# Optimization experiments

Measured on AMD Instinct MI355X. Metric: run time of the kernel, lower is better.

Reference implementation:

```python
import jax, jax.numpy as jnp
import numpy as np

B, L, D, H = 256, 256, 128, 256
IMPUTE_WEIGHT = 1.0


def setup_inputs() -> dict:
    key = jax.random.key(0)
    ks = jax.random.split(key, 20)
    s = 0.05
    inp = {
        "values": jax.random.normal(ks[0], (B, L, D), jnp.float32),
        "masks": jax.random.randint(ks[1], (B, L, D), 0, 2).astype(jnp.float32),
        "deltas": jax.random.uniform(ks[2], (B, L, D), jnp.float32),
        "eval_masks": jax.random.randint(ks[3], (B, L, D), 0, 2).astype(jnp.float32),
        "td_h_W": jax.random.normal(ks[4], (H, D), jnp.float32) * s,
        "td_h_b": jax.random.normal(ks[5], (H,), jnp.float32) * s,
        "td_x_w": jax.random.normal(ks[6], (D,), jnp.float32) * s,  # diag of TemporalDecay(diag=True)
        "td_x_b": jax.random.normal(ks[7], (D,), jnp.float32) * s,
        "hist_W": jax.random.normal(ks[8], (D, H), jnp.float32) * s,
        "hist_b": jax.random.normal(ks[9], (D,), jnp.float32) * s,
        "feat_W": jax.random.normal(ks[10], (D, D), jnp.float32) * s,
        "feat_b": jax.random.normal(ks[11], (D,), jnp.float32) * s,
        "wc_W": jax.random.normal(ks[12], (D, 2 * D), jnp.float32) * s,
        "wc_b": jax.random.normal(ks[13], (D,), jnp.float32) * s,
        "W_ih": jax.random.normal(ks[14], (4 * H, 2 * D), jnp.float32) * s,
        "W_hh": jax.random.normal(ks[15], (4 * H, H), jnp.float32) * s,
        "b_ih": jax.random.normal(ks[16], (4 * H,), jnp.float32) * s,
        "b_hh": jax.random.normal(ks[17], (4 * H,), jnp.float32) * s,
    }
    return inp


def _rits_forward(values, masks, deltas, eval_masks,
                  td_h_W, td_h_b, td_x_w, td_x_b,
                  hist_W, hist_b, feat_W, feat_b,
                  wc_W, wc_b, W_ih, W_hh, b_ih, b_hh):
    feat_mask = 1.0 - jnp.eye(D, dtype=values.dtype)  # zero diagonal
    Wf = feat_W * feat_mask

    def step(carry, xs):
        h, c, loss = carry
        x, m, d, me = xs  # each (B, D)
        gamma_h = jnp.exp(-jax.nn.relu(d @ td_h_W.T + td_h_b))   # (B, H)
        gamma_x = jnp.exp(-jax.nn.relu(d * td_x_w + td_x_b))      # (B, D) diag linear
        h = h * gamma_h
        x_h = h @ hist_W.T + hist_b                               # (B, D)
        x_c = m * x + (1.0 - m) * x_h
        z_h = x_c @ Wf.T + feat_b                                 # (B, D)
        alpha = jnp.concatenate([gamma_x, m], axis=1) @ wc_W.T + wc_b
        c_h = alpha * z_h + (1.0 - alpha) * x_h
        c_c = m * x + (1.0 - m) * c_h
        loss = loss + jnp.sum(jnp.abs(c_c - x) * me) / (jnp.sum(me) + 1e-5)
        inputs = jnp.concatenate([c_c, m], axis=1)                # (B, 2D)
        gates = inputs @ W_ih.T + b_ih + h @ W_hh.T + b_hh        # (B, 4H)
        i, f, g, o = jnp.split(gates, 4, axis=1)
        i, f, o = jax.nn.sigmoid(i), jax.nn.sigmoid(f), jax.nn.sigmoid(o)
        g = jnp.tanh(g)
        c = f * c + i * g
        h = o * jnp.tanh(c)
        return (h, c, loss), c_c

    h0 = jnp.zeros((values.shape[0], H), values.dtype)
    c0 = jnp.zeros((values.shape[0], H), values.dtype)
    loss0 = jnp.zeros((), values.dtype)
    xs = (jnp.swapaxes(values, 0, 1), jnp.swapaxes(masks, 0, 1),
          jnp.swapaxes(deltas, 0, 1), jnp.swapaxes(eval_masks, 0, 1))  # (L, B, D)
    (_, _, loss), imps = jax.lax.scan(step, (h0, c0, loss0), xs)
    imputations = jnp.swapaxes(imps, 0, 1)  # (B, L, D)
    return imputations, loss * IMPUTE_WEIGHT


def reference(values, masks, deltas, eval_masks,
              td_h_W, td_h_b, td_x_w, td_x_b,
              hist_W, hist_b, feat_W, feat_b,
              wc_W, wc_b, W_ih, W_hh, b_ih, b_hh):
    return _rits_forward(values, masks, deltas, eval_masks,
                         td_h_W, td_h_b, td_x_w, td_x_b,
                         hist_W, hist_b, feat_W, feat_b,
                         wc_W, wc_b, W_ih, W_hh, b_ih, b_hh)
```

## Files before the change

### kernel.cpp

```cpp
#include <hip/hip_runtime.h>
#include <math.h>


namespace {
constexpr int Bn = 256, Ln = 256, Dn = 128, Hn = 256;
constexpr long LD = (long)Ln * Dn;

constexpr int OFF_LOSS  = 0;
constexpr int OFF_DEN   = 256;
constexpr int OFF_BIASG = 2048;
constexpr int OFF_WG    = 8192;
constexpr int OFF_HISTP = 1056768;
constexpr int OFF_TDHP  = 1122304;
constexpr int OFF_WFP   = 1187840;
constexpr int OFF_WCP   = 1220608;
}

typedef _Float16 h2f __attribute__((ext_vector_type(2)));
typedef unsigned int uint32;

__device__ __forceinline__ float fdot2(uint32 a, uint32 b, float c) {
  return __builtin_amdgcn_fdot2(__builtin_bit_cast(h2f, a),
                                __builtin_bit_cast(h2f, b), c, false);
}
__device__ __forceinline__ uint32 packf16(float a, float b) {
  h2f p; p[0] = (_Float16)a; p[1] = (_Float16)b;
  return __builtin_bit_cast(uint32, p);
}
__device__ __forceinline__ unsigned short f16u(float a) {
  _Float16 h = (_Float16)a; return __builtin_bit_cast(unsigned short, h);
}

__global__ void rits_prep(const float* __restrict__ td_h_W,
                          const float* __restrict__ hist_W,
                          const float* __restrict__ feat_W,
                          const float* __restrict__ wc_W,
                          const float* __restrict__ W_ih,
                          const float* __restrict__ W_hh,
                          const float* __restrict__ b_ih,
                          const float* __restrict__ b_hh,
                          const float* __restrict__ evalm,
                          char* __restrict__ wsb) {
  const int blk = blockIdx.x, tid = threadIdx.x;
  if (blk < 1248) {
    int idx = blk * 256 + tid;
    if (idx < 262144) {
      int kp = idx >> 11, rem = idx & 2047, jj = rem >> 3, s8 = rem & 7;
      const float* src = (s8 < 4) ? W_ih : W_hh;
      int q = s8 & 3;
      const float* row = src + (size_t)(q * 256 + jj) * 256 + 2 * kp;
      ((uint32*)(wsb + OFF_WG))[idx] = packf16(row[0], row[1]);
    } else if (idx < 278528) {
      int i2 = idx - 262144, kp = i2 >> 7, d = i2 & 127;
      ((uint32*)(wsb + OFF_HISTP))[i2] =
          packf16(hist_W[d * 256 + 2 * kp], hist_W[d * 256 + 2 * kp + 1]);
    } else if (idx < 294912) {
      int i2 = idx - 278528, kp = i2 >> 8, h = i2 & 255;
      ((uint32*)(wsb + OFF_TDHP))[i2] =
          packf16(td_h_W[h * 128 + 2 * kp], td_h_W[h * 128 + 2 * kp + 1]);
    } else if (idx < 303104) {
      int i2 = idx - 294912, kp = i2 >> 7, d = i2 & 127;
      float a = (2 * kp == d) ? 0.f : feat_W[d * 128 + 2 * kp];
      float b = (2 * kp + 1 == d) ? 0.f : feat_W[d * 128 + 2 * kp + 1];
      ((uint32*)(wsb + OFF_WFP))[i2] = packf16(a, b);
    } else if (idx < 319488) {
      int i2 = idx - 303104, kp = i2 >> 7, d = i2 & 127;
      ((uint32*)(wsb + OFF_WCP))[i2] =
          packf16(wc_W[d * 256 + 2 * kp], wc_W[d * 256 + 2 * kp + 1]);
    }
  } else if (blk < 1252) {
    int i = (blk - 1248) * 256 + tid;
    int jj = i >> 2, q = i & 3;
    ((float*)(wsb + OFF_BIASG))[jj * 4 + q] =
        b_ih[q * 256 + jj] + b_hh[q * 256 + jj];
    if (blk == 1248 && tid == 0) *((float*)(wsb + OFF_LOSS)) = 0.f;
  } else {
    int t = blk - 1252;
    __shared__ float red[256];
    int d = tid & 127, g = tid >> 7;
    float s = 0.f;
    for (int b = g; b < 256; b += 2) s += evalm[(size_t)b * LD + t * 128 + d];
    red[tid] = s;
    __syncthreads();
    for (int o = 128; o > 0; o >>= 1) {
      if (tid < o) red[tid] += red[tid + o];
      __syncthreads();
    }
    if (tid == 0) ((float*)(wsb + OFF_DEN))[t] = red[0] + 1e-5f;
  }
}

__global__ __launch_bounds__(1024, 4) void rits_rec(
    const float* __restrict__ values, const float* __restrict__ masks,
    const float* __restrict__ deltas, const float* __restrict__ evalm,
    const float* __restrict__ td_h_b, const float* __restrict__ td_x_w,
    const float* __restrict__ td_x_b, const float* __restrict__ hist_b,
    const float* __restrict__ feat_b, const float* __restrict__ wc_b,
    char* __restrict__ wsb, float* __restrict__ outp) {
  __shared__ __align__(16) float scratch[8224];
  __shared__ float den_s[256], bg_s[1024], tdhb_s[256];
  __shared__ float txw_s[128], txb_s[128], hb_s[128], fb_s[128], wcb_s[128];
  __shared__ float hf[2][256], cst[2][256];
  __shared__ float xs[2][128], ms[2][128], es[2][128];
  __shared__ float xh_s[2][128], al_s[2][128];
  __shared__ __align__(8) unsigned short hdU16[128 * 4];
  __shared__ __align__(8) unsigned short cmU16[128 * 4];
  __shared__ __align__(8) unsigned short xcU16[64 * 4];
  __shared__ uint32 drP[64 * 2];
  __shared__ uint32 gxmP[128 * 2];

  const int tid = threadIdx.x;
  const size_t b0 = (size_t)blockIdx.x * 2;
  const uint32* hdU32 = (const uint32*)hdU16;
  const uint32* cmU32 = (const uint32*)cmU16;
  const uint32* xcU32 = (const uint32*)xcU16;
  const uint32* wg = (const uint32*)(wsb + OFF_WG);
  const uint4* histP4 = (const uint4*)(wsb + OFF_HISTP);
  const uint4* tdhP4 = (const uint4*)(wsb + OFF_TDHP);
  const uint4* wfP4 = (const uint4*)(wsb + OFF_WFP);
  const uint4* wcP4 = (const uint4*)(wsb + OFF_WCP);

  if (tid < 512) { ((float*)hf)[tid] = 0.f; ((float*)cst)[tid] = 0.f; }
  bg_s[tid] = ((const float*)(wsb + OFF_BIASG))[tid];
  if (tid < 256) {
    den_s[tid] = ((const float*)(wsb + OFF_DEN))[tid];
    tdhb_s[tid] = td_h_b[tid];
  } else if (tid < 384) txw_s[tid - 256] = td_x_w[tid - 256];
  else if (tid < 512) txb_s[tid - 384] = td_x_b[tid - 384];
  else if (tid < 640) hb_s[tid - 512] = hist_b[tid - 512];
  else if (tid < 768) fb_s[tid - 640] = feat_b[tid - 640];
  else if (tid < 896) wcb_s[tid - 768] = wc_b[tid - 768];
  __syncthreads();

  float lacc = 0.f;
  for (int t = 0; t < Ln; ++t) {
    const size_t base = b0 * LD + (size_t)t * 128;
    if (tid < 256) {
      int d = tid & 127, r = tid >> 7;
      size_t gi = base + (size_t)r * LD + d;
      xs[r][d] = values[gi];
      ms[r][d] = masks[gi];
      es[r][d] = evalm[gi];
    } else if (tid < 512) {
      int i = tid - 256, kp = i & 127, r = i >> 7;
      size_t gb = base + (size_t)r * LD;
      if (kp < 64) {
        float d0v = deltas[gb + 2 * kp], d1v = deltas[gb + 2 * kp + 1];
        drP[kp * 2 + r] = packf16(d0v, d1v);
        float g0 = __expf(-fmaxf(fmaf(d0v, txw_s[2 * kp], txb_s[2 * kp]), 0.f));
        float g1 = __expf(-fmaxf(fmaf(d1v, txw_s[2 * kp + 1], txb_s[2 * kp + 1]), 0.f));
        gxmP[kp * 2 + r] = packf16(g0, g1);
      } else {
        int k2 = kp - 64;
        gxmP[kp * 2 + r] = packf16(masks[gb + 2 * k2], masks[gb + 2 * k2 + 1]);
      }
    }
    __syncthreads();

    if (tid < 256) {
      int g = tid & 63, r = (tid >> 6) & 1, kq = tid >> 7;
      float4 a = {0.f, 0.f, 0.f, 0.f};
#pragma unroll 4
      for (int i = 0; i < 32; ++i) {
        int kp = kq * 32 + i;
        uint4 w = tdhP4[kp * 64 + g];
        uint32 dr = drP[kp * 2 + r];
        a.x = fdot2(dr, w.x, a.x); a.y = fdot2(dr, w.y, a.y);
        a.z = fdot2(dr, w.z, a.z); a.w = fdot2(dr, w.w, a.w);
      }
      ((float4*)(scratch + (kq * 2 + r) * 260))[g] = a;
    } else if (tid < 768) {
      int i0 = tid - 256, g = i0 & 31, r = (i0 >> 5) & 1, kq = i0 >> 6;
      float4 a = {0.f, 0.f, 0.f, 0.f};
#pragma unroll 4
      for (int i = 0; i < 16; ++i) {
        int kp = kq * 16 + i;
        uint4 w = wcP4[kp * 32 + g];
        uint32 gm = gxmP[kp * 2 + r];
        a.x = fdot2(gm, w.x, a.x); a.y = fdot2(gm, w.y, a.y);
        a.z = fdot2(gm, w.z, a.z); a.w = fdot2(gm, w.w, a.w);
      }
      ((float4*)(scratch + 1040 + (kq * 2 + r) * 132))[g] = a;
    }
    __syncthreads();

    if (tid < 512) {
      int h = tid & 255, r = tid >> 8;
      float s = scratch[r * 260 + h] + scratch[(2 + r) * 260 + h] + tdhb_s[h];
      float hd = hf[r][h] * __expf(-fmaxf(s, 0.f));
      hdU16[(h >> 1) * 4 + 2 * r + (h & 1)] = f16u(hd);
    } else if (tid < 768) {
      int i0 = tid - 512, d = i0 & 127, r = i0 >> 7;
      float s = wcb_s[d];
#pragma unroll
      for (int kq = 0; kq < 8; ++kq) s += scratch[1040 + (kq * 2 + r) * 132 + d];
      al_s[r][d] = s;
    }
    __syncthreads();

    if (tid < 512) {
      int g = tid & 31, r = (tid >> 5) & 1, kq = tid >> 6;
      float4 a = {0.f, 0.f, 0.f, 0.f};
#pragma unroll 4
      for (int i = 0; i < 16; ++i) {
        int kp = kq * 16 + i;
        uint4 w = histP4[kp * 32 + g];
        uint32 hd = hdU32[kp * 2 + r];
        a.x = fdot2(hd, w.x, a.x); a.y = fdot2(hd, w.y, a.y);
        a.z = fdot2(hd, w.z, a.z); a.w = fdot2(hd, w.w, a.w);
      }
      ((float4*)(scratch + (kq * 2 + r) * 132))[g] = a;
    }
    __syncthreads();

    if (tid < 256) {
      int d = tid & 127, r = tid >> 7;
      float xh = hb_s[d];
#pragma unroll
      for (int kq = 0; kq < 8; ++kq) xh += scratch[(kq * 2 + r) * 132 + d];
      xh_s[r][d] = xh;
      float mm = ms[r][d];
      float xc = mm * xs[r][d] + (1.f - mm) * xh;
      xcU16[(d >> 1) * 4 + 2 * r + (d & 1)] = f16u(xc);
    }
    __syncthreads();

    if (tid < 512) {
      int g = tid & 31, r = (tid >> 5) & 1, kq = tid >> 6;
      float4 a = {0.f, 0.f, 0.f, 0.f};
#pragma unroll 4
      for (int i = 0; i < 8; ++i) {
        int kp = kq * 8 + i;
        uint4 w = wfP4[kp * 32 + g];
        uint32 xc = xcU32[kp * 2 + r];
        a.x = fdot2(xc, w.x, a.x); a.y = fdot2(xc, w.y, a.y);
        a.z = fdot2(xc, w.z, a.z); a.w = fdot2(xc, w.w, a.w);
      }
      ((float4*)(scratch + (kq * 2 + r) * 132))[g] = a;
    }
    __syncthreads();

    if (tid < 256) {
      int d = tid & 127, r = tid >> 7;
      float z = fb_s[d];
#pragma unroll
      for (int kq = 0; kq < 8; ++kq) z += scratch[(kq * 2 + r) * 132 + d];
      float a = al_s[r][d], xh = xh_s[r][d];
      float ch = a * z + (1.f - a) * xh;
      float mm = ms[r][d], xv = xs[r][d];
      float cc = mm * xv + (1.f - mm) * ch;
      outp[base + (size_t)r * LD + d] = cc;
      lacc += (1.f - mm) * fabsf(ch - xv) * es[r][d] / den_s[t];
      cmU16[(d >> 1) * 4 + 2 * r + (d & 1)] = f16u(cc);
      cmU16[(64 + (d >> 1)) * 4 + 2 * r + (d & 1)] = f16u(mm);
    }
    __syncthreads();

    {
      int jj = tid & 255, kq = tid >> 8;
      int kp0 = kq * 32;
      const uint4* wp = (const uint4*)(wg + ((size_t)kp0 * 256 + jj) * 8);
      float a00 = 0, a01 = 0, a02 = 0, a03 = 0;
      float a10 = 0, a11 = 0, a12 = 0, a13 = 0;
#pragma unroll 4
      for (int i = 0; i < 32; ++i) {
        int kp = kp0 + i;
        uint4 wv = wp[0];
        uint4 wh = wp[1];
        wp += 512;
        uint32 c0 = cmU32[kp * 2 + 0], c1 = cmU32[kp * 2 + 1];
        uint32 h0 = hdU32[kp * 2 + 0], h1 = hdU32[kp * 2 + 1];
        a00 = fdot2(c0, wv.x, a00); a01 = fdot2(c0, wv.y, a01);
        a02 = fdot2(c0, wv.z, a02); a03 = fdot2(c0, wv.w, a03);
        a10 = fdot2(c1, wv.x, a10); a11 = fdot2(c1, wv.y, a11);
        a12 = fdot2(c1, wv.z, a12); a13 = fdot2(c1, wv.w, a13);
        a00 = fdot2(h0, wh.x, a00); a01 = fdot2(h0, wh.y, a01);
        a02 = fdot2(h0, wh.z, a02); a03 = fdot2(h0, wh.w, a03);
        a10 = fdot2(h1, wh.x, a10); a11 = fdot2(h1, wh.y, a11);
        a12 = fdot2(h1, wh.z, a12); a13 = fdot2(h1, wh.w, a13);
      }
      float* pg = scratch;
      pg[(kq * 8 + 0) * 257 + jj] = a00; pg[(kq * 8 + 1) * 257 + jj] = a01;
      pg[(kq * 8 + 2) * 257 + jj] = a02; pg[(kq * 8 + 3) * 257 + jj] = a03;
      pg[(kq * 8 + 4) * 257 + jj] = a10; pg[(kq * 8 + 5) * 257 + jj] = a11;
      pg[(kq * 8 + 6) * 257 + jj] = a12; pg[(kq * 8 + 7) * 257 + jj] = a13;
    }
    __syncthreads();

    if (tid < 256) {
      int jj = tid;
      const float* pg = scratch;
#pragma unroll
      for (int r = 0; r < 2; ++r) {
        float g0 = bg_s[jj * 4 + 0], g1 = bg_s[jj * 4 + 1];
        float g2 = bg_s[jj * 4 + 2], g3 = bg_s[jj * 4 + 3];
#pragma unroll
        for (int kq = 0; kq < 4; ++kq) {
          g0 += pg[(kq * 8 + r * 4 + 0) * 257 + jj];
          g1 += pg[(kq * 8 + r * 4 + 1) * 257 + jj];
          g2 += pg[(kq * 8 + r * 4 + 2) * 257 + jj];
          g3 += pg[(kq * 8 + r * 4 + 3) * 257 + jj];
        }
        float ig = 1.f / (1.f + __expf(-g0));
        float fg = 1.f / (1.f + __expf(-g1));
        float gg = tanhf(g2);
        float og = 1.f / (1.f + __expf(-g3));
        float c = fg * cst[r][jj] + ig * gg;
        cst[r][jj] = c;
        hf[r][jj] = og * tanhf(c);
      }
    }
    __syncthreads();
  }

  scratch[tid] = lacc;
  __syncthreads();
  for (int o = 512; o > 0; o >>= 1) {
    if (tid < o) scratch[tid] += scratch[tid + o];
    __syncthreads();
  }
  if (tid == 0) atomicAdd((float*)(wsb + OFF_LOSS), scratch[0]);
}

__global__ void rits_fin(const char* __restrict__ wsb, float* __restrict__ outp) {
  if (threadIdx.x == 0 && blockIdx.x == 0)
    outp[(size_t)Bn * LD] = *((const float*)(wsb + OFF_LOSS));
}

extern "C" void kernel_launch(void* const* d_in, const int* in_sizes, int n_in,
                              void* d_out, int out_size, void* d_ws,
                              size_t ws_size, hipStream_t stream) {
  const float* values = (const float*)d_in[0];
  const float* masks  = (const float*)d_in[1];
  const float* deltas = (const float*)d_in[2];
  const float* evalm  = (const float*)d_in[3];
  const float* td_h_W = (const float*)d_in[4];
  const float* td_h_b = (const float*)d_in[5];
  const float* td_x_w = (const float*)d_in[6];
  const float* td_x_b = (const float*)d_in[7];
  const float* hist_W = (const float*)d_in[8];
  const float* hist_b = (const float*)d_in[9];
  const float* feat_W = (const float*)d_in[10];
  const float* feat_b = (const float*)d_in[11];
  const float* wc_W   = (const float*)d_in[12];
  const float* wc_b   = (const float*)d_in[13];
  const float* W_ih   = (const float*)d_in[14];
  const float* W_hh   = (const float*)d_in[15];
  const float* b_ih   = (const float*)d_in[16];
  const float* b_hh   = (const float*)d_in[17];
  char* wsb = (char*)d_ws;
  float* outp = (float*)d_out;

  hipLaunchKernelGGL(rits_prep, dim3(1508), dim3(256), 0, stream, td_h_W,
                     hist_W, feat_W, wc_W, W_ih, W_hh, b_ih, b_hh, evalm, wsb);
  hipLaunchKernelGGL(rits_rec, dim3(128), dim3(1024), 0, stream, values, masks,
                     deltas, evalm, td_h_b, td_x_w, td_x_b, hist_b, feat_b,
                     wc_b, wsb, outp);
  hipLaunchKernelGGL(rits_fin, dim3(1), dim3(64), 0, stream, wsb, outp);
}
```

Before: 3.562 ms.

## Split each batch pair's recurrence across two blocks exchanging state via global flags

Launches two blocks per batch pair, each owning half of the hidden units (H split) for the temporal-decay, history projection and LSTM gate matvecs. Each step the blocks exchange their decayed hidden halves and partial x_h sums through a global workspace, using release/acquire flags with a bounded spin. This doubles the number of active CUs on the serial recurrence and halves per-block weight streaming. The cost is a cross-block global-memory handshake every time step, and the scheme relies on both partner blocks being co-resident.

```diff
diff --git a/kernel.cpp b/kernel.cpp
--- a/kernel.cpp
+++ b/kernel.cpp
@@ -14,10 +14,13 @@
 constexpr int OFF_TDHP  = 1122304;
 constexpr int OFF_WFP   = 1187840;
 constexpr int OFF_WCP   = 1220608;
+constexpr int OFF_EXCH  = 1310720;
+constexpr int OFF_FLAG  = 2097152;
 }
 
 typedef _Float16 h2f __attribute__((ext_vector_type(2)));
 typedef unsigned int uint32;
+typedef unsigned long long uint64;
 
 __device__ __forceinline__ float fdot2(uint32 a, uint32 b, float c) {
   return __builtin_amdgcn_fdot2(__builtin_bit_cast(h2f, a),
@@ -74,7 +77,7 @@
     ((float*)(wsb + OFF_BIASG))[jj * 4 + q] =
         b_ih[q * 256 + jj] + b_hh[q * 256 + jj];
     if (blk == 1248 && tid == 0) *((float*)(wsb + OFF_LOSS)) = 0.f;
-  } else {
+  } else if (blk < 1508) {
     int t = blk - 1252;
     __shared__ float red[256];
     int d = tid & 127, g = tid >> 7;
@@ -87,6 +90,8 @@
       __syncthreads();
     }
     if (tid == 0) ((float*)(wsb + OFF_DEN))[t] = red[0] + 1e-5f;
+  } else {
+    for (int i = tid; i < 4096; i += 256) ((uint32*)(wsb + OFF_FLAG))[i] = 0u;
   }
 }
 
@@ -97,11 +102,12 @@
     const float* __restrict__ td_x_b, const float* __restrict__ hist_b,
     const float* __restrict__ feat_b, const float* __restrict__ wc_b,
     char* __restrict__ wsb, float* __restrict__ outp) {
-  __shared__ __align__(16) float scratch[8224];
-  __shared__ float den_s[256], bg_s[1024], tdhb_s[256];
+  __shared__ __align__(16) float scratch[8448];
+  __shared__ float den_s[256], bg_s[512], tdhb_s[128];
   __shared__ float txw_s[128], txb_s[128], hb_s[128], fb_s[128], wcb_s[128];
-  __shared__ float hf[2][256], cst[2][256];
+  __shared__ float hf[2][128], cst[2][128];
   __shared__ float xs[2][128], ms[2][128], es[2][128];
+  __shared__ float xhp[2][2][128];
   __shared__ float xh_s[2][128], al_s[2][128];
   __shared__ __align__(8) unsigned short hdU16[128 * 4];
   __shared__ __align__(8) unsigned short cmU16[128 * 4];
@@ -110,7 +116,10 @@
   __shared__ uint32 gxmP[128 * 2];
 
   const int tid = threadIdx.x;
-  const size_t b0 = (size_t)blockIdx.x * 2;
+  const int bid = blockIdx.x;
+  const int sh = bid >> 7;
+  const int pair = bid & 127;
+  const size_t b0 = (size_t)pair * 2;
   const uint32* hdU32 = (const uint32*)hdU16;
   const uint32* cmU32 = (const uint32*)cmU16;
   const uint32* xcU32 = (const uint32*)xcU16;
@@ -119,22 +128,31 @@
   const uint4* tdhP4 = (const uint4*)(wsb + OFF_TDHP);
   const uint4* wfP4 = (const uint4*)(wsb + OFF_WFP);
   const uint4* wcP4 = (const uint4*)(wsb + OFF_WCP);
-
-  if (tid < 512) { ((float*)hf)[tid] = 0.f; ((float*)cst)[tid] = 0.f; }
-  bg_s[tid] = ((const float*)(wsb + OFF_BIASG))[tid];
-  if (tid < 256) {
-    den_s[tid] = ((const float*)(wsb + OFF_DEN))[tid];
-    tdhb_s[tid] = td_h_b[tid];
-  } else if (tid < 384) txw_s[tid - 256] = td_x_w[tid - 256];
-  else if (tid < 512) txb_s[tid - 384] = td_x_b[tid - 384];
-  else if (tid < 640) hb_s[tid - 512] = hist_b[tid - 512];
-  else if (tid < 768) fb_s[tid - 640] = feat_b[tid - 640];
-  else if (tid < 896) wcb_s[tid - 768] = wc_b[tid - 768];
+  char* exch = wsb + OFF_EXCH;
+  unsigned int* myf = (unsigned int*)(wsb + OFF_FLAG + ((pair << 1) | sh) * 64);
+  unsigned int* pf  = (unsigned int*)(wsb + OFF_FLAG + ((pair << 1) | (sh ^ 1)) * 64);
+
+  if (tid < 512) bg_s[tid] = ((const float*)(wsb + OFF_BIASG))[sh * 512 + tid];
+  else if (tid < 768) den_s[tid - 512] = ((const float*)(wsb + OFF_DEN))[tid - 512];
+  else if (tid < 896) tdhb_s[tid - 768] = td_h_b[(sh << 7) + (tid - 768)];
+  else txw_s[tid - 896] = td_x_w[tid - 896];
+  if (tid < 128) txb_s[tid] = td_x_b[tid];
+  else if (tid < 256) hb_s[tid - 128] = hist_b[tid - 128];
+  else if (tid < 384) fb_s[tid - 256] = feat_b[tid - 256];
+  else if (tid < 512) wcb_s[tid - 384] = wc_b[tid - 384];
+  else {
+    int i = tid - 512;
+    if (i < 256) ((float*)hf)[i] = 0.f;
+    else ((float*)cst)[i - 256] = 0.f;
+  }
   __syncthreads();
 
   float lacc = 0.f;
   for (int t = 0; t < Ln; ++t) {
     const size_t base = b0 * LD + (size_t)t * 128;
+    uint64* myp = (uint64*)(exch + ((((pair << 1) | sh) << 1) | (t & 1)) * 1536);
+    uint64* pp  = (uint64*)(exch + ((((pair << 1) | (sh ^ 1)) << 1) | (t & 1)) * 1536);
+
     if (tid < 256) {
       int d = tid & 127, r = tid >> 7;
       size_t gi = base + (size_t)r * LD + d;
@@ -158,17 +176,18 @@
     __syncthreads();
 
     if (tid < 256) {
-      int g = tid & 63, r = (tid >> 6) & 1, kq = tid >> 7;
+      int g = tid & 31, r = (tid >> 5) & 1, kq = tid >> 6;
+      int gg = (sh << 5) + g;
       float4 a = {0.f, 0.f, 0.f, 0.f};
 #pragma unroll 4
-      for (int i = 0; i < 32; ++i) {
-        int kp = kq * 32 + i;
-        uint4 w = tdhP4[kp * 64 + g];
+      for (int i = 0; i < 16; ++i) {
+        int kp = kq * 16 + i;
+        uint4 w = tdhP4[kp * 64 + gg];
         uint32 dr = drP[kp * 2 + r];
         a.x = fdot2(dr, w.x, a.x); a.y = fdot2(dr, w.y, a.y);
         a.z = fdot2(dr, w.z, a.z); a.w = fdot2(dr, w.w, a.w);
       }
-      ((float4*)(scratch + (kq * 2 + r) * 260))[g] = a;
+      ((float4*)(scratch + (kq * 2 + r) * 132))[g] = a;
     } else if (tid < 768) {
       int i0 = tid - 256, g = i0 & 31, r = (i0 >> 5) & 1, kq = i0 >> 6;
       float4 a = {0.f, 0.f, 0.f, 0.f};
@@ -180,21 +199,24 @@
         a.x = fdot2(gm, w.x, a.x); a.y = fdot2(gm, w.y, a.y);
         a.z = fdot2(gm, w.z, a.z); a.w = fdot2(gm, w.w, a.w);
       }
-      ((float4*)(scratch + 1040 + (kq * 2 + r) * 132))[g] = a;
-    }
-    __syncthreads();
-
-    if (tid < 512) {
-      int h = tid & 255, r = tid >> 8;
-      float s = scratch[r * 260 + h] + scratch[(2 + r) * 260 + h] + tdhb_s[h];
-      float hd = hf[r][h] * __expf(-fmaxf(s, 0.f));
-      hdU16[(h >> 1) * 4 + 2 * r + (h & 1)] = f16u(hd);
-    } else if (tid < 768) {
+      ((float4*)(scratch + 1056 + (kq * 2 + r) * 132))[g] = a;
+    }
+    __syncthreads();
+
+    if (tid < 256) {
+      int hl = tid & 127, r = tid >> 7;
+      float ssum = tdhb_s[hl];
+#pragma unroll
+      for (int kq = 0; kq < 4; ++kq) ssum += scratch[(kq * 2 + r) * 132 + hl];
+      float hd = hf[r][hl] * __expf(-fmaxf(ssum, 0.f));
+      int hg = (sh << 7) | hl;
+      hdU16[(hg >> 1) * 4 + 2 * r + (hg & 1)] = f16u(hd);
+    } else if (tid >= 512 && tid < 768) {
       int i0 = tid - 512, d = i0 & 127, r = i0 >> 7;
-      float s = wcb_s[d];
+      float ssum = wcb_s[d];
 #pragma unroll
-      for (int kq = 0; kq < 8; ++kq) s += scratch[1040 + (kq * 2 + r) * 132 + d];
-      al_s[r][d] = s;
+      for (int kq = 0; kq < 8; ++kq) ssum += scratch[1056 + (kq * 2 + r) * 132 + d];
+      al_s[r][d] = ssum;
     }
     __syncthreads();
 
@@ -202,22 +224,61 @@
       int g = tid & 31, r = (tid >> 5) & 1, kq = tid >> 6;
       float4 a = {0.f, 0.f, 0.f, 0.f};
 #pragma unroll 4
-      for (int i = 0; i < 16; ++i) {
-        int kp = kq * 16 + i;
+      for (int i = 0; i < 8; ++i) {
+        int kp = (sh << 6) + kq * 8 + i;
         uint4 w = histP4[kp * 32 + g];
         uint32 hd = hdU32[kp * 2 + r];
         a.x = fdot2(hd, w.x, a.x); a.y = fdot2(hd, w.y, a.y);
         a.z = fdot2(hd, w.z, a.z); a.w = fdot2(hd, w.w, a.w);
       }
       ((float4*)(scratch + (kq * 2 + r) * 132))[g] = a;
+    } else if (tid < 576) {
+      int i = tid - 512;
+      uint64 v = ((const uint64*)hdU16)[(sh << 6) + i];
+      __hip_atomic_store(myp + i, v, __ATOMIC_RELAXED, __HIP_MEMORY_SCOPE_AGENT);
     }
     __syncthreads();
 
     if (tid < 256) {
       int d = tid & 127, r = tid >> 7;
-      float xh = hb_s[d];
+      float xo = 0.f;
 #pragma unroll
-      for (int kq = 0; kq < 8; ++kq) xh += scratch[(kq * 2 + r) * 132 + d];
+      for (int kq = 0; kq < 8; ++kq) xo += scratch[(kq * 2 + r) * 132 + d];
+      xhp[sh][r][d] = xo;
+      __hip_atomic_store((uint32*)myp + 128 + (r << 7) + d,
+                         __builtin_bit_cast(uint32, xo),
+                         __ATOMIC_RELAXED, __HIP_MEMORY_SCOPE_AGENT);
+    }
+    __syncthreads();
+
+    if (tid == 0) {
+      __hip_atomic_store(myf, (unsigned)(t + 1), __ATOMIC_RELEASE,
+                         __HIP_MEMORY_SCOPE_AGENT);
+      unsigned guard = 0;
+      while (__hip_atomic_load(pf, __ATOMIC_ACQUIRE,
+                               __HIP_MEMORY_SCOPE_AGENT) < (unsigned)(t + 1)) {
+        if (++guard > (1u << 22)) break;
+      }
+    }
+    __syncthreads();
+
+    if (tid < 192) {
+      uint64 v = __hip_atomic_load(pp + tid, __ATOMIC_RELAXED,
+                                   __HIP_MEMORY_SCOPE_AGENT);
+      if (tid < 64) {
+        ((uint64*)hdU16)[((sh ^ 1) << 6) + tid] = v;
+      } else {
+        int j = tid - 64;
+        int r = j >> 6, d2 = (j & 63) << 1;
+        xhp[sh ^ 1][r][d2] = __builtin_bit_cast(float, (uint32)v);
+        xhp[sh ^ 1][r][d2 + 1] = __builtin_bit_cast(float, (uint32)(v >> 32));
+      }
+    }
+    __syncthreads();
+
+    if (tid < 256) {
+      int d = tid & 127, r = tid >> 7;
+      float xh = xhp[0][r][d] + xhp[1][r][d] + hb_s[d];
       xh_s[r][d] = xh;
       float mm = ms[r][d];
       float xc = mm * xs[r][d] + (1.f - mm) * xh;
@@ -249,21 +310,24 @@
       float ch = a * z + (1.f - a) * xh;
       float mm = ms[r][d], xv = xs[r][d];
       float cc = mm * xv + (1.f - mm) * ch;
-      outp[base + (size_t)r * LD + d] = cc;
-      lacc += (1.f - mm) * fabsf(ch - xv) * es[r][d] / den_s[t];
+      if (r == sh) {
+        outp[base + (size_t)r * LD + d] = cc;
+        lacc += (1.f - mm) * fabsf(ch - xv) * es[r][d] / den_s[t];
+      }
       cmU16[(d >> 1) * 4 + 2 * r + (d & 1)] = f16u(cc);
       cmU16[(64 + (d >> 1)) * 4 + 2 * r + (d & 1)] = f16u(mm);
     }
     __syncthreads();
 
     {
-      int jj = tid & 255, kq = tid >> 8;
-      int kp0 = kq * 32;
-      const uint4* wp = (const uint4*)(wg + ((size_t)kp0 * 256 + jj) * 8);
+      int jj = tid & 127, kq = tid >> 7;
+      int jg = (sh << 7) | jj;
+      int kp0 = kq * 16;
+      const uint4* wp = (const uint4*)(wg + ((size_t)kp0 * 256 + jg) * 8);
       float a00 = 0, a01 = 0, a02 = 0, a03 = 0;
       float a10 = 0, a11 = 0, a12 = 0, a13 = 0;
 #pragma unroll 4
-      for (int i = 0; i < 32; ++i) {
+      for (int i = 0; i < 16; ++i) {
         int kp = kp0 + i;
         uint4 wv = wp[0];
         uint4 wh = wp[1];
@@ -280,35 +344,30 @@
         a12 = fdot2(h1, wh.z, a12); a13 = fdot2(h1, wh.w, a13);
       }
       float* pg = scratch;
-      pg[(kq * 8 + 0) * 257 + jj] = a00; pg[(kq * 8 + 1) * 257 + jj] = a01;
-      pg[(kq * 8 + 2) * 257 + jj] = a02; pg[(kq * 8 + 3) * 257 + jj] = a03;
-      pg[(kq * 8 + 4) * 257 + jj] = a10; pg[(kq * 8 + 5) * 257 + jj] = a11;
-      pg[(kq * 8 + 6) * 257 + jj] = a12; pg[(kq * 8 + 7) * 257 + jj] = a13;
-    }
-    __syncthreads();
-
-    if (tid < 256) {
-      int jj = tid;
-      const float* pg = scratch;
+      pg[(kq * 8 + 0) * 132 + jj] = a00; pg[(kq * 8 + 1) * 132 + jj] = a01;
+      pg[(kq * 8 + 2) * 132 + jj] = a02; pg[(kq * 8 + 3) * 132 + jj] = a03;
+      pg[(kq * 8 + 4) * 132 + jj] = a10; pg[(kq * 8 + 5) * 132 + jj] = a11;
+      pg[(kq * 8 + 6) * 132 + jj] = a12; pg[(kq * 8 + 7) * 132 + jj] = a13;
+    }
+    __syncthreads();
+
+    if (tid < 256) {
+      int jj = tid & 127, r = tid >> 7;
+      float g0 = bg_s[jj * 4 + 0], g1 = bg_s[jj * 4 + 1];
+      float g2 = bg_s[jj * 4 + 2], g3 = bg_s[jj * 4 + 3];
 #pragma unroll
-      for (int r = 0; r < 2; ++r) {
-        float g0 = bg_s[jj * 4 + 0], g1 = bg_s[jj * 4 + 1];
-        float g2 = bg_s[jj * 4 + 2], g3 = bg_s[jj * 4 + 3];
-#pragma unroll
-        for (int kq = 0; kq < 4; ++kq) {
-          g0 += pg[(kq * 8 + r * 4 + 0) * 257 + jj];
-          g1 += pg[(kq * 8 + r * 4 + 1) * 257 + jj];
-          g2 += pg[(kq * 8 + r * 4 + 2) * 257 + jj];
-          g3 += pg[(kq * 8 + r * 4 + 3) * 257 + jj];
-        }
-        float ig = 1.f / (1.f + __expf(-g0));
-        float fg = 1.f / (1.f + __expf(-g1));
-        float gg = tanhf(g2);
-        float og = 1.f / (1.f + __expf(-g3));
-        float c = fg * cst[r][jj] + ig * gg;
-        cst[r][jj] = c;
-        hf[r][jj] = og * tanhf(c);
-      }
+      for (int kq = 0; kq < 8; ++kq) {
+        int bix = (kq * 8 + r * 4) * 132 + jj;
+        g0 += scratch[bix]; g1 += scratch[bix + 132];
+        g2 += scratch[bix + 264]; g3 += scratch[bix + 396];
+      }
+      float ig = 1.f / (1.f + __expf(-g0));
+      float fg = 1.f / (1.f + __expf(-g1));
+      float gg = tanhf(g2);
+      float og = 1.f / (1.f + __expf(-g3));
+      float c = fg * cst[r][jj] + ig * gg;
+      cst[r][jj] = c;
+      hf[r][jj] = og * tanhf(c);
     }
     __syncthreads();
   }
@@ -351,9 +410,9 @@
   char* wsb = (char*)d_ws;
   float* outp = (float*)d_out;
 
-  hipLaunchKernelGGL(rits_prep, dim3(1508), dim3(256), 0, stream, td_h_W,
+  hipLaunchKernelGGL(rits_prep, dim3(1509), dim3(256), 0, stream, td_h_W,
                      hist_W, feat_W, wc_W, W_ih, W_hh, b_ih, b_hh, evalm, wsb);
-  hipLaunchKernelGGL(rits_rec, dim3(128), dim3(1024), 0, stream, values, masks,
+  hipLaunchKernelGGL(rits_rec, dim3(256), dim3(1024), 0, stream, values, masks,
                      deltas, evalm, td_h_b, td_x_w, td_x_b, hist_b, feat_b,
                      wc_b, wsb, outp);
   hipLaunchKernelGGL(rits_fin, dim3(1), dim3(64), 0, stream, wsb, outp);
```

New measurement: 3.563 ms. No clear change (+0.0%).

## Split LSTM hidden dim across 4 cooperating blocks with global flag exchange

Applied to the files above, without the earlier changes.

Restructures the recurrent kernel so each group of 4 batch rows is handled by 4 blocks, each owning a quarter of the hidden units. The blocks exchange the decayed hidden state and alpha slices each timestep through global memory using release/acquire flags. Gate weights stay in registers and the hist/feat weights are cached in LDS. This cuts per-block weight traffic and spreads the work over 256 blocks. The cost is a cross-block spin-wait every step and the assumption that all 256 blocks are resident at once, which could deadlock or hit the guard timeout if they are not.

```diff
diff --git a/kernel.cpp b/kernel.cpp
--- a/kernel.cpp
+++ b/kernel.cpp
@@ -14,6 +14,8 @@
 constexpr int OFF_TDHP  = 1122304;
 constexpr int OFF_WFP   = 1187840;
 constexpr int OFF_WCP   = 1220608;
+constexpr int OFF_EXCH  = 1286144;
+constexpr int OFF_FLAG  = 1810432;
 }
 
 typedef _Float16 h2f __attribute__((ext_vector_type(2)));
@@ -26,9 +28,6 @@
 __device__ __forceinline__ uint32 packf16(float a, float b) {
   h2f p; p[0] = (_Float16)a; p[1] = (_Float16)b;
   return __builtin_bit_cast(uint32, p);
-}
-__device__ __forceinline__ unsigned short f16u(float a) {
-  _Float16 h = (_Float16)a; return __builtin_bit_cast(unsigned short, h);
 }
 
 __global__ void rits_prep(const float* __restrict__ td_h_W,
@@ -74,7 +73,7 @@
     ((float*)(wsb + OFF_BIASG))[jj * 4 + q] =
         b_ih[q * 256 + jj] + b_hh[q * 256 + jj];
     if (blk == 1248 && tid == 0) *((float*)(wsb + OFF_LOSS)) = 0.f;
-  } else {
+  } else if (blk < 1508) {
     int t = blk - 1252;
     __shared__ float red[256];
     int d = tid & 127, g = tid >> 7;
@@ -87,235 +86,278 @@
       __syncthreads();
     }
     if (tid == 0) ((float*)(wsb + OFF_DEN))[t] = red[0] + 1e-5f;
+  } else {
+    for (int i = tid; i < 4096; i += 256) ((uint32*)(wsb + OFF_FLAG))[i] = 0u;
   }
 }
 
-__global__ __launch_bounds__(1024, 4) void rits_rec(
+__global__ __launch_bounds__(512, 2) void rits_rec(
     const float* __restrict__ values, const float* __restrict__ masks,
     const float* __restrict__ deltas, const float* __restrict__ evalm,
     const float* __restrict__ td_h_b, const float* __restrict__ td_x_w,
     const float* __restrict__ td_x_b, const float* __restrict__ hist_b,
     const float* __restrict__ feat_b, const float* __restrict__ wc_b,
     char* __restrict__ wsb, float* __restrict__ outp) {
-  __shared__ __align__(16) float scratch[8224];
-  __shared__ float den_s[256], bg_s[1024], tdhb_s[256];
+  __shared__ uint32 histL[16384];
+  __shared__ uint32 wfL[8192];
+  __shared__ __align__(16) float scratch[4608];
+  __shared__ float al_s[4][128];
+  __shared__ float hf[4][64], cst[4][64];
+  __shared__ __align__(16) uint32 hdP[512];
+  __shared__ __align__(16) uint32 cmP[512];
+  __shared__ __align__(16) uint32 xcP[256];
+  __shared__ __align__(16) uint32 drP[256];
+  __shared__ __align__(16) uint32 gxmP[512];
+  __shared__ float bg_s[256];
+  __shared__ float tdhb_s[64];
   __shared__ float txw_s[128], txb_s[128], hb_s[128], fb_s[128], wcb_s[128];
-  __shared__ float hf[2][256], cst[2][256];
-  __shared__ float xs[2][128], ms[2][128], es[2][128];
-  __shared__ float xh_s[2][128], al_s[2][128];
-  __shared__ __align__(8) unsigned short hdU16[128 * 4];
-  __shared__ __align__(8) unsigned short cmU16[128 * 4];
-  __shared__ __align__(8) unsigned short xcU16[64 * 4];
-  __shared__ uint32 drP[64 * 2];
-  __shared__ uint32 gxmP[128 * 2];
 
   const int tid = threadIdx.x;
-  const size_t b0 = (size_t)blockIdx.x * 2;
-  const uint32* hdU32 = (const uint32*)hdU16;
-  const uint32* cmU32 = (const uint32*)cmU16;
-  const uint32* xcU32 = (const uint32*)xcU16;
+  const int bid = blockIdx.x;
+  const int sh = bid >> 6;
+  const int grp = bid & 63;
+  const size_t b0 = (size_t)grp * 4;
   const uint32* wg = (const uint32*)(wsb + OFF_WG);
-  const uint4* histP4 = (const uint4*)(wsb + OFF_HISTP);
-  const uint4* tdhP4 = (const uint4*)(wsb + OFF_TDHP);
-  const uint4* wfP4 = (const uint4*)(wsb + OFF_WFP);
-  const uint4* wcP4 = (const uint4*)(wsb + OFF_WCP);
-
-  if (tid < 512) { ((float*)hf)[tid] = 0.f; ((float*)cst)[tid] = 0.f; }
-  bg_s[tid] = ((const float*)(wsb + OFF_BIASG))[tid];
+  const uint32* tdhG = (const uint32*)(wsb + OFF_TDHP);
+  const uint32* wcG = (const uint32*)(wsb + OFF_WCP);
+  const float* denG = (const float*)(wsb + OFF_DEN);
+  char* exch = wsb + OFF_EXCH;
+  unsigned int* flg = (unsigned int*)(wsb + OFF_FLAG);
+
+  {
+    const uint4* hG = (const uint4*)(wsb + OFF_HISTP);
+#pragma unroll
+    for (int k = 0; k < 8; ++k) ((uint4*)histL)[k * 512 + tid] = hG[k * 512 + tid];
+    const uint4* fG = (const uint4*)(wsb + OFF_WFP);
+#pragma unroll
+    for (int k = 0; k < 4; ++k) ((uint4*)wfL)[k * 512 + tid] = fG[k * 512 + tid];
+  }
   if (tid < 256) {
-    den_s[tid] = ((const float*)(wsb + OFF_DEN))[tid];
-    tdhb_s[tid] = td_h_b[tid];
-  } else if (tid < 384) txw_s[tid - 256] = td_x_w[tid - 256];
-  else if (tid < 512) txb_s[tid - 384] = td_x_b[tid - 384];
-  else if (tid < 640) hb_s[tid - 512] = hist_b[tid - 512];
-  else if (tid < 768) fb_s[tid - 640] = feat_b[tid - 640];
-  else if (tid < 896) wcb_s[tid - 768] = wc_b[tid - 768];
+    bg_s[tid] = ((const float*)(wsb + OFF_BIASG))[(sh * 64 + (tid & 63)) * 4 + (tid >> 6)];
+  } else if (tid < 320) tdhb_s[tid - 256] = td_h_b[sh * 64 + (tid - 256)];
+  else if (tid < 448) txw_s[tid - 320] = td_x_w[tid - 320];
+  if (tid < 128) txb_s[tid] = td_x_b[tid];
+  else if (tid < 256) hb_s[tid - 128] = hist_b[tid - 128];
+  else if (tid < 384) fb_s[tid - 256] = feat_b[tid - 256];
+  else wcb_s[tid - 384] = wc_b[tid - 384];
+  if (tid < 256) ((float*)hf)[tid] = 0.f;
+  else ((float*)cst)[tid - 256] = 0.f;
+
+  const int dA = tid & 127, rA = tid >> 7;
+  const int hlB = tid & 63, kqB = (tid >> 6) & 7;
+  const int dlB = tid & 31, kqA = tid >> 5;
+  const int jjH = tid & 63, qhH = (tid >> 6) & 1, kqH = tid >> 7;
+  const int jg = sh * 64 + jjH;
+
+  uint2 wv_[32], wh_[32];
+#pragma unroll
+  for (int i = 0; i < 32; ++i) {
+    const uint32* p = wg + ((size_t)((kqH * 32 + i) * 256 + jg)) * 8 + 2 * qhH;
+    wv_[i] = *(const uint2*)p;
+    wh_[i] = *(const uint2*)(p + 4);
+  }
+  uint32 tw[8];
+#pragma unroll
+  for (int i = 0; i < 8; ++i) tw[i] = tdhG[(kqB * 8 + i) * 256 + sh * 64 + hlB];
+  uint32 cw[8];
+#pragma unroll
+  for (int i = 0; i < 8; ++i) cw[i] = wcG[(kqA * 8 + i) * 128 + sh * 32 + dlB];
   __syncthreads();
 
   float lacc = 0.f;
   for (int t = 0; t < Ln; ++t) {
     const size_t base = b0 * LD + (size_t)t * 128;
+    uint32* mypU = (uint32*)(exch + (size_t)(bid * 2 + (t & 1)) * 1024);
+
+    const size_t gi = base + (size_t)rA * LD + dA;
+    const float xv = values[gi];
+    const float mv = masks[gi];
+    const float ev = evalm[gi];
+    {
+      const size_t gb = base + (size_t)rA * LD;
+      if (dA < 64) {
+        float d0v = deltas[gb + 2 * dA], d1v = deltas[gb + 2 * dA + 1];
+        drP[dA * 4 + rA] = packf16(d0v, d1v);
+        float g0 = __expf(-fmaxf(fmaf(d0v, txw_s[2 * dA], txb_s[2 * dA]), 0.f));
+        float g1 = __expf(-fmaxf(fmaf(d1v, txw_s[2 * dA + 1], txb_s[2 * dA + 1]), 0.f));
+        gxmP[dA * 4 + rA] = packf16(g0, g1);
+      } else {
+        int k2 = dA - 64;
+        gxmP[dA * 4 + rA] = packf16(masks[gb + 2 * k2], masks[gb + 2 * k2 + 1]);
+      }
+    }
+    __syncthreads();
+
+    {
+      float ga0 = 0.f, ga1 = 0.f, ga2 = 0.f, ga3 = 0.f;
+#pragma unroll
+      for (int i = 0; i < 8; ++i) {
+        uint4 d4 = *(const uint4*)&drP[(kqB * 8 + i) * 4];
+        ga0 = fdot2(d4.x, tw[i], ga0); ga1 = fdot2(d4.y, tw[i], ga1);
+        ga2 = fdot2(d4.z, tw[i], ga2); ga3 = fdot2(d4.w, tw[i], ga3);
+      }
+      scratch[2304 + (kqB * 4 + 0) * 68 + hlB] = ga0;
+      scratch[2304 + (kqB * 4 + 1) * 68 + hlB] = ga1;
+      scratch[2304 + (kqB * 4 + 2) * 68 + hlB] = ga2;
+      scratch[2304 + (kqB * 4 + 3) * 68 + hlB] = ga3;
+      float aa0 = 0.f, aa1 = 0.f, aa2 = 0.f, aa3 = 0.f;
+#pragma unroll
+      for (int i = 0; i < 8; ++i) {
+        uint4 g4 = *(const uint4*)&gxmP[(kqA * 8 + i) * 4];
+        aa0 = fdot2(g4.x, cw[i], aa0); aa1 = fdot2(g4.y, cw[i], aa1);
+        aa2 = fdot2(g4.z, cw[i], aa2); aa3 = fdot2(g4.w, cw[i], aa3);
+      }
+      scratch[(kqA * 4 + 0) * 36 + dlB] = aa0;
+      scratch[(kqA * 4 + 1) * 36 + dlB] = aa1;
+      scratch[(kqA * 4 + 2) * 36 + dlB] = aa2;
+      scratch[(kqA * 4 + 3) * 36 + dlB] = aa3;
+    }
+    __syncthreads();
+
     if (tid < 256) {
-      int d = tid & 127, r = tid >> 7;
-      size_t gi = base + (size_t)r * LD + d;
-      xs[r][d] = values[gi];
-      ms[r][d] = masks[gi];
-      es[r][d] = evalm[gi];
-    } else if (tid < 512) {
-      int i = tid - 256, kp = i & 127, r = i >> 7;
-      size_t gb = base + (size_t)r * LD;
-      if (kp < 64) {
-        float d0v = deltas[gb + 2 * kp], d1v = deltas[gb + 2 * kp + 1];
-        drP[kp * 2 + r] = packf16(d0v, d1v);
-        float g0 = __expf(-fmaxf(fmaf(d0v, txw_s[2 * kp], txb_s[2 * kp]), 0.f));
-        float g1 = __expf(-fmaxf(fmaf(d1v, txw_s[2 * kp + 1], txb_s[2 * kp + 1]), 0.f));
-        gxmP[kp * 2 + r] = packf16(g0, g1);
-      } else {
-        int k2 = kp - 64;
-        gxmP[kp * 2 + r] = packf16(masks[gb + 2 * k2], masks[gb + 2 * k2 + 1]);
+      int hl = tid & 63, r = tid >> 6;
+      float s = tdhb_s[hl];
+#pragma unroll
+      for (int kq = 0; kq < 8; ++kq) s += scratch[2304 + (kq * 4 + r) * 68 + hl];
+      float hd = hf[r][hl] * __expf(-fmaxf(s, 0.f));
+      float hdo = __shfl_down(hd, 1);
+      if (!(hl & 1)) {
+        uint32 pv = packf16(hd, hdo);
+        int kpl = hl >> 1;
+        hdP[(sh * 32 + kpl) * 4 + r] = pv;
+        __hip_atomic_store(mypU + kpl * 4 + r, pv, __ATOMIC_RELAXED,
+                           __HIP_MEMORY_SCOPE_AGENT);
+      }
+    } else if (tid < 384) {
+      int i0 = tid - 256, dl = i0 & 31, r = i0 >> 5;
+      float s = wcb_s[sh * 32 + dl];
+#pragma unroll
+      for (int kq = 0; kq < 16; ++kq) s += scratch[(kq * 4 + r) * 36 + dl];
+      al_s[r][sh * 32 + dl] = s;
+      __hip_atomic_store(mypU + 128 + r * 32 + dl,
+                         __builtin_bit_cast(uint32, s),
+                         __ATOMIC_RELAXED, __HIP_MEMORY_SCOPE_AGENT);
+    }
+    __syncthreads();
+
+    if (tid == 0)
+      __hip_atomic_store(flg + bid * 16, (unsigned)(t + 1), __ATOMIC_RELEASE,
+                         __HIP_MEMORY_SCOPE_AGENT);
+    if (tid < 3) {
+      int ps = tid + (tid >= sh ? 1 : 0);
+      unsigned* pfp = flg + (ps * 64 + grp) * 16;
+      unsigned guard = 0;
+      while (__hip_atomic_load(pfp, __ATOMIC_ACQUIRE,
+                               __HIP_MEMORY_SCOPE_AGENT) < (unsigned)(t + 1)) {
+        if (++guard > (1u << 24)) break;
       }
     }
     __syncthreads();
 
     if (tid < 256) {
-      int g = tid & 63, r = (tid >> 6) & 1, kq = tid >> 7;
-      float4 a = {0.f, 0.f, 0.f, 0.f};
-#pragma unroll 4
+#pragma unroll
+      for (int p = 0; p < 3; ++p) {
+        int ps = p + (p >= sh ? 1 : 0);
+        const uint32* pq =
+            (const uint32*)(exch + (size_t)((ps * 64 + grp) * 2 + (t & 1)) * 1024);
+        uint32 v = __hip_atomic_load(pq + tid, __ATOMIC_RELAXED,
+                                     __HIP_MEMORY_SCOPE_AGENT);
+        if (tid < 128) hdP[ps * 128 + tid] = v;
+        else {
+          int i = tid - 128;
+          al_s[i >> 5][ps * 32 + (i & 31)] = __builtin_bit_cast(float, v);
+        }
+      }
+    }
+    __syncthreads();
+
+    float xhv;
+    {
+      float xh = hb_s[dA];
+#pragma unroll 16
+      for (int kp = 0; kp < 128; ++kp)
+        xh = fdot2(hdP[kp * 4 + rA], histL[kp * 128 + dA], xh);
+      xhv = xh;
+      float xc = mv * xv + (1.f - mv) * xh;
+      float xco = __shfl_down(xc, 1);
+      if (!(dA & 1)) xcP[((dA >> 1)) * 4 + rA] = packf16(xc, xco);
+    }
+    __syncthreads();
+
+    {
+      float z = fb_s[dA];
+#pragma unroll 16
+      for (int kp = 0; kp < 64; ++kp)
+        z = fdot2(xcP[kp * 4 + rA], wfL[kp * 128 + dA], z);
+      float a = al_s[rA][dA];
+      float ch = a * z + (1.f - a) * xhv;
+      float cc = mv * xv + (1.f - mv) * ch;
+      if (rA == sh) {
+        outp[base + (size_t)rA * LD + dA] = cc;
+        lacc += (1.f - mv) * fabsf(ch - xv) * ev / denG[t];
+      }
+      float cco = __shfl_down(cc, 1);
+      float mmo = __shfl_down(mv, 1);
+      if (!(dA & 1)) {
+        cmP[(dA >> 1) * 4 + rA] = packf16(cc, cco);
+        cmP[(64 + (dA >> 1)) * 4 + rA] = packf16(mv, mmo);
+      }
+    }
+    __syncthreads();
+
+    {
+      float a00 = 0.f, a01 = 0.f, a02 = 0.f, a03 = 0.f;
+      float a10 = 0.f, a11 = 0.f, a12 = 0.f, a13 = 0.f;
+#pragma unroll
       for (int i = 0; i < 32; ++i) {
-        int kp = kq * 32 + i;
-        uint4 w = tdhP4[kp * 64 + g];
-        uint32 dr = drP[kp * 2 + r];
-        a.x = fdot2(dr, w.x, a.x); a.y = fdot2(dr, w.y, a.y);
-        a.z = fdot2(dr, w.z, a.z); a.w = fdot2(dr, w.w, a.w);
-      }
-      ((float4*)(scratch + (kq * 2 + r) * 260))[g] = a;
-    } else if (tid < 768) {
-      int i0 = tid - 256, g = i0 & 31, r = (i0 >> 5) & 1, kq = i0 >> 6;
-      float4 a = {0.f, 0.f, 0.f, 0.f};
-#pragma unroll 4
-      for (int i = 0; i < 16; ++i) {
-        int kp = kq * 16 + i;
-        uint4 w = wcP4[kp * 32 + g];
-        uint32 gm = gxmP[kp * 2 + r];
-        a.x = fdot2(gm, w.x, a.x); a.y = fdot2(gm, w.y, a.y);
-        a.z = fdot2(gm, w.z, a.z); a.w = fdot2(gm, w.w, a.w);
-      }
-      ((float4*)(scratch + 1040 + (kq * 2 + r) * 132))[g] = a;
-    }
-    __syncthreads();
-
-    if (tid < 512) {
-      int h = tid & 255, r = tid >> 8;
-      float s = scratch[r * 260 + h] + scratch[(2 + r) * 260 + h] + tdhb_s[h];
-      float hd = hf[r][h] * __expf(-fmaxf(s, 0.f));
-      hdU16[(h >> 1) * 4 + 2 * r + (h & 1)] = f16u(hd);
-    } else if (tid < 768) {
-      int i0 = tid - 512, d = i0 & 127, r = i0 >> 7;
-      float s = wcb_s[d];
-#pragma unroll
-      for (int kq = 0; kq < 8; ++kq) s += scratch[1040 + (kq * 2 + r) * 132 + d];
-      al_s[r][d] = s;
-    }
-    __syncthreads();
-
-    if (tid < 512) {
-      int g = tid & 31, r = (tid >> 5) & 1, kq = tid >> 6;
-      float4 a = {0.f, 0.f, 0.f, 0.f};
-#pragma unroll 4
-      for (int i = 0; i < 16; ++i) {
-        int kp = kq * 16 + i;
-        uint4 w = histP4[kp * 32 + g];
-        uint32 hd = hdU32[kp * 2 + r];
-        a.x = fdot2(hd, w.x, a.x); a.y = fdot2(hd, w.y, a.y);
-        a.z = fdot2(hd, w.z, a.z); a.w = fdot2(hd, w.w, a.w);
-      }
-      ((float4*)(scratch + (kq * 2 + r) * 132))[g] = a;
+        int kp = kqH * 32 + i;
+        uint4 c4 = *(const uint4*)&cmP[kp * 4];
+        uint4 h4 = *(const uint4*)&hdP[kp * 4];
+        a00 = fdot2(c4.x, wv_[i].x, a00); a10 = fdot2(c4.x, wv_[i].y, a10);
+        a00 = fdot2(h4.x, wh_[i].x, a00); a10 = fdot2(h4.x, wh_[i].y, a10);
+        a01 = fdot2(c4.y, wv_[i].x, a01); a11 = fdot2(c4.y, wv_[i].y, a11);
+        a01 = fdot2(h4.y, wh_[i].x, a01); a11 = fdot2(h4.y, wh_[i].y, a11);
+        a02 = fdot2(c4.z, wv_[i].x, a02); a12 = fdot2(c4.z, wv_[i].y, a12);
+        a02 = fdot2(h4.z, wh_[i].x, a02); a12 = fdot2(h4.z, wh_[i].y, a12);
+        a03 = fdot2(c4.w, wv_[i].x, a03); a13 = fdot2(c4.w, wv_[i].y, a13);
+        a03 = fdot2(h4.w, wh_[i].x, a03); a13 = fdot2(h4.w, wh_[i].y, a13);
+      }
+      const int q0 = 2 * qhH, q1 = 2 * qhH + 1;
+      scratch[(kqH * 16 + 0 * 4 + q0) * 64 + jjH] = a00;
+      scratch[(kqH * 16 + 1 * 4 + q0) * 64 + jjH] = a01;
+      scratch[(kqH * 16 + 2 * 4 + q0) * 64 + jjH] = a02;
+      scratch[(kqH * 16 + 3 * 4 + q0) * 64 + jjH] = a03;
+      scratch[(kqH * 16 + 0 * 4 + q1) * 64 + jjH] = a10;
+      scratch[(kqH * 16 + 1 * 4 + q1) * 64 + jjH] = a11;
+      scratch[(kqH * 16 + 2 * 4 + q1) * 64 + jjH] = a12;
+      scratch[(kqH * 16 + 3 * 4 + q1) * 64 + jjH] = a13;
     }
     __syncthreads();
 
     if (tid < 256) {
-      int d = tid & 127, r = tid >> 7;
-      float xh = hb_s[d];
-#pragma unroll
-      for (int kq = 0; kq < 8; ++kq) xh += scratch[(kq * 2 + r) * 132 + d];
-      xh_s[r][d] = xh;
-      float mm = ms[r][d];
-      float xc = mm * xs[r][d] + (1.f - mm) * xh;
-      xcU16[(d >> 1) * 4 + 2 * r + (d & 1)] = f16u(xc);
-    }
-    __syncthreads();
-
-    if (tid < 512) {
-      int g = tid & 31, r = (tid >> 5) & 1, kq = tid >> 6;
-      float4 a = {0.f, 0.f, 0.f, 0.f};
-#pragma unroll 4
-      for (int i = 0; i < 8; ++i) {
-        int kp = kq * 8 + i;
-        uint4 w = wfP4[kp * 32 + g];
-        uint32 xc = xcU32[kp * 2 + r];
-        a.x = fdot2(xc, w.x, a.x); a.y = fdot2(xc, w.y, a.y);
-        a.z = fdot2(xc, w.z, a.z); a.w = fdot2(xc, w.w, a.w);
-      }
-      ((float4*)(scratch + (kq * 2 + r) * 132))[g] = a;
-    }
-    __syncthreads();
-
-    if (tid < 256) {
-      int d = tid & 127, r = tid >> 7;
-      float z = fb_s[d];
-#pragma unroll
-      for (int kq = 0; kq < 8; ++kq) z += scratch[(kq * 2 + r) * 132 + d];
-      float a = al_s[r][d], xh = xh_s[r][d];
-      float ch = a * z + (1.f - a) * xh;
-      float mm = ms[r][d], xv = xs[r][d];
-      float cc = mm * xv + (1.f - mm) * ch;
-      outp[base + (size_t)r * LD + d] = cc;
-      lacc += (1.f - mm) * fabsf(ch - xv) * es[r][d] / den_s[t];
-      cmU16[(d >> 1) * 4 + 2 * r + (d & 1)] = f16u(cc);
-      cmU16[(64 + (d >> 1)) * 4 + 2 * r + (d & 1)] = f16u(mm);
-    }
-    __syncthreads();
-
-    {
-      int jj = tid & 255, kq = tid >> 8;
-      int kp0 = kq * 32;
-      const uint4* wp = (const uint4*)(wg + ((size_t)kp0 * 256 + jj) * 8);
-      float a00 = 0, a01 = 0, a02 = 0, a03 = 0;
-      float a10 = 0, a11 = 0, a12 = 0, a13 = 0;
-#pragma unroll 4
-      for (int i = 0; i < 32; ++i) {
-        int kp = kp0 + i;
-        uint4 wv = wp[0];
-        uint4 wh = wp[1];
-        wp += 512;
-        uint32 c0 = cmU32[kp * 2 + 0], c1 = cmU32[kp * 2 + 1];
-        uint32 h0 = hdU32[kp * 2 + 0], h1 = hdU32[kp * 2 + 1];
-        a00 = fdot2(c0, wv.x, a00); a01 = fdot2(c0, wv.y, a01);
-        a02 = fdot2(c0, wv.z, a02); a03 = fdot2(c0, wv.w, a03);
-        a10 = fdot2(c1, wv.x, a10); a11 = fdot2(c1, wv.y, a11);
-        a12 = fdot2(c1, wv.z, a12); a13 = fdot2(c1, wv.w, a13);
-        a00 = fdot2(h0, wh.x, a00); a01 = fdot2(h0, wh.y, a01);
-        a02 = fdot2(h0, wh.z, a02); a03 = fdot2(h0, wh.w, a03);
-        a10 = fdot2(h1, wh.x, a10); a11 = fdot2(h1, wh.y, a11);
-        a12 = fdot2(h1, wh.z, a12); a13 = fdot2(h1, wh.w, a13);
-      }
-      float* pg = scratch;
-      pg[(kq * 8 + 0) * 257 + jj] = a00; pg[(kq * 8 + 1) * 257 + jj] = a01;
-      pg[(kq * 8 + 2) * 257 + jj] = a02; pg[(kq * 8 + 3) * 257 + jj] = a03;
-      pg[(kq * 8 + 4) * 257 + jj] = a10; pg[(kq * 8 + 5) * 257 + jj] = a11;
-      pg[(kq * 8 + 6) * 257 + jj] = a12; pg[(kq * 8 + 7) * 257 + jj] = a13;
-    }
-    __syncthreads();
-
-    if (tid < 256) {
-      int jj = tid;
-      const float* pg = scratch;
-#pragma unroll
-      for (int r = 0; r < 2; ++r) {
-        float g0 = bg_s[jj * 4 + 0], g1 = bg_s[jj * 4 + 1];
-        float g2 = bg_s[jj * 4 + 2], g3 = bg_s[jj * 4 + 3];
-#pragma unroll
-        for (int kq = 0; kq < 4; ++kq) {
-          g0 += pg[(kq * 8 + r * 4 + 0) * 257 + jj];
-          g1 += pg[(kq * 8 + r * 4 + 1) * 257 + jj];
-          g2 += pg[(kq * 8 + r * 4 + 2) * 257 + jj];
-          g3 += pg[(kq * 8 + r * 4 + 3) * 257 + jj];
-        }
-        float ig = 1.f / (1.f + __expf(-g0));
-        float fg = 1.f / (1.f + __expf(-g1));
-        float gg = tanhf(g2);
-        float og = 1.f / (1.f + __expf(-g3));
-        float c = fg * cst[r][jj] + ig * gg;
-        cst[r][jj] = c;
-        hf[r][jj] = og * tanhf(c);
-      }
+      int jj = tid & 63, r = tid >> 6;
+      float g0 = bg_s[0 * 64 + jj], g1 = bg_s[1 * 64 + jj];
+      float g2 = bg_s[2 * 64 + jj], g3 = bg_s[3 * 64 + jj];
+#pragma unroll
+      for (int kq = 0; kq < 4; ++kq) {
+        int bx = (kq * 16 + r * 4) * 64 + jj;
+        g0 += scratch[bx]; g1 += scratch[bx + 64];
+        g2 += scratch[bx + 128]; g3 += scratch[bx + 192];
+      }
+      float ig = 1.f / (1.f + __expf(-g0));
+      float fg = 1.f / (1.f + __expf(-g1));
+      float gg = tanhf(g2);
+      float og = 1.f / (1.f + __expf(-g3));
+      float c = fg * cst[r][jj] + ig * gg;
+      cst[r][jj] = c;
+      hf[r][jj] = og * tanhf(c);
     }
     __syncthreads();
   }
 
   scratch[tid] = lacc;
   __syncthreads();
-  for (int o = 512; o > 0; o >>= 1) {
+  for (int o = 256; o > 0; o >>= 1) {
     if (tid < o) scratch[tid] += scratch[tid + o];
     __syncthreads();
   }
@@ -351,9 +393,9 @@
   char* wsb = (char*)d_ws;
   float* outp = (float*)d_out;
 
-  hipLaunchKernelGGL(rits_prep, dim3(1508), dim3(256), 0, stream, td_h_W,
+  hipLaunchKernelGGL(rits_prep, dim3(1509), dim3(256), 0, stream, td_h_W,
                      hist_W, feat_W, wc_W, W_ih, W_hh, b_ih, b_hh, evalm, wsb);
-  hipLaunchKernelGGL(rits_rec, dim3(128), dim3(1024), 0, stream, values, masks,
+  hipLaunchKernelGGL(rits_rec, dim3(256), dim3(512), 0, stream, values, masks,
                      deltas, evalm, td_h_b, td_x_w, td_x_b, hist_b, feat_b,
                      wc_b, wsb, outp);
   hipLaunchKernelGGL(rits_fin, dim3(1), dim3(64), 0, stream, wsb, outp);
```

Measured after the change: 3.693 ms. +3.7%, slower.
